# Kernel optimization log

Measured on AMD Instinct MI355X. Metric: run time of the kernel, lower is better.

## Reference

```python
import jax, jax.numpy as jnp
import numpy as np


def gcn_conv(x, W, b, src, dst):
    """PyG-style GCNConv: add self-loops, symmetric normalization, then scatter-add."""
    n = x.shape[0]
    loop = jnp.arange(n, dtype=src.dtype)
    s = jnp.concatenate([src, loop])  # [E+N]
    d = jnp.concatenate([dst, loop])
    deg = jax.ops.segment_sum(jnp.ones(s.shape[0], dtype=x.dtype), d, num_segments=n)
    dinv = jax.lax.rsqrt(jnp.maximum(deg, 1.0))  # deg >= 1 due to self-loops
    norm = dinv[s] * dinv[d]                     # [E+N]
    h = x @ W                                    # [N, out]
    msg = h[s] * norm[:, None]                   # gather + scale
    return jax.ops.segment_sum(msg, d, num_segments=n) + b


def setup_inputs() -> dict:
    key = jax.random.key(0)
    ks = jax.random.split(key, 8)
    N, E, IN, H, C = 50000, 800000, 128, 64, 16
    x = jax.random.normal(ks[0], (N, IN), dtype=jnp.float32)
    edge_index = jax.random.randint(ks[1], (2, E), 0, N, dtype=jnp.int32)
    def glorot(k, shp):
        fan_in, fan_out = shp
        lim = (6.0 / (fan_in + fan_out)) ** 0.5
        return jax.random.uniform(k, shp, jnp.float32, -lim, lim)
    return {
        "x": x,
        "edge_index": edge_index,
        "W1": glorot(ks[2], (IN, H)), "b1": jnp.zeros((H,), jnp.float32),
        "W2": glorot(ks[3], (H, H)),  "b2": jnp.zeros((H,), jnp.float32),
        "Wm1": glorot(ks[4], (2 * H, H)), "bm1": jnp.zeros((H,), jnp.float32),
        "Wm2": glorot(ks[5], (H, C)),     "bm2": jnp.zeros((C,), jnp.float32),
    }


def reference(x, edge_index, W1, b1, W2, b2, Wm1, bm1, Wm2, bm2):
    src, dst = edge_index[0], edge_index[1]
    h = jax.nn.relu(gcn_conv(x, W1, b1, src, dst))
    # dropout is identity in eval mode
    h = jax.nn.relu(gcn_conv(h, W2, b2, src, dst))
    ef = jnp.concatenate([h[src], h[dst]], axis=1)  # [E, 2H]
    z = jax.nn.relu(ef @ Wm1 + bm1)
    return z @ Wm2 + bm2  # [E, numClasses]
```

## Files before the change

### kernel.cpp

```cpp
#include <hip/hip_runtime.h>
#include <hip/hip_bf16.h>

__global__ __launch_bounds__(256) void k_deg(const int* __restrict__ dst, int* __restrict__ deg, int E) {
    int e = blockIdx.x * 256 + threadIdx.x;
    if (e < E) atomicAdd(&deg[dst[e]], 1);
}

__global__ __launch_bounds__(256) void k_dinv(const int* __restrict__ deg, float* __restrict__ dinv, int N) {
    int n = blockIdx.x * 256 + threadIdx.x;
    if (n < N) dinv[n] = rsqrtf((float)(deg[n] + 1));
}

__global__ __launch_bounds__(256) void k_scan_sum(const int* __restrict__ deg, int* __restrict__ bsum, int N) {
    int n = blockIdx.x * 256 + threadIdx.x;
    int v = (n < N) ? deg[n] : 0;
#pragma unroll
    for (int o = 32; o > 0; o >>= 1) v += __shfl_down(v, o, 64);
    __shared__ int sh[4];
    if ((threadIdx.x & 63) == 0) sh[threadIdx.x >> 6] = v;
    __syncthreads();
    if (threadIdx.x == 0) bsum[blockIdx.x] = sh[0] + sh[1] + sh[2] + sh[3];
}

__global__ __launch_bounds__(256) void k_scan_off(int* __restrict__ bsum, int nb) {
    __shared__ int sh[256];
    int t = threadIdx.x;
    sh[t] = (t < nb) ? bsum[t] : 0;
    __syncthreads();
    for (int o = 1; o < 256; o <<= 1) {
        int y = (t >= o) ? sh[t - o] : 0;
        __syncthreads();
        sh[t] += y;
        __syncthreads();
    }
    if (t < nb) bsum[t] = (t == 0) ? 0 : sh[t - 1];
}

__global__ __launch_bounds__(256) void k_scan_write(const int* __restrict__ deg, const int* __restrict__ boff,
                                                    int* __restrict__ row_start, int* __restrict__ cursor, int N) {
    int n = blockIdx.x * 256 + threadIdx.x;
    int t = threadIdx.x, lane = t & 63, w = t >> 6;
    int v = (n < N) ? deg[n] : 0;
    int x = v;
#pragma unroll
    for (int o = 1; o < 64; o <<= 1) {
        int y = __shfl_up(x, o, 64);
        if (lane >= o) x += y;
    }
    __shared__ int wsum[4];
    if (lane == 63) wsum[w] = x;
    __syncthreads();
    int wo = 0;
#pragma unroll
    for (int i = 0; i < 4; ++i) wo += (i < w) ? wsum[i] : 0;
    int excl = boff[blockIdx.x] + wo + x - v;
    if (n < N) { row_start[n] = excl; cursor[n] = excl; }
    if (n == N - 1) row_start[N] = excl + v;
}

template <bool PAIR>
__global__ __launch_bounds__(256) void k_fill(const int* __restrict__ src, const int* __restrict__ dst,
                                              int* __restrict__ cursor, void* __restrict__ item, int E) {
    int e = blockIdx.x * 256 + threadIdx.x;
    if (e < E) {
        int d = dst[e];
        int pos = atomicAdd(&cursor[d], 1);
        if (PAIR) ((int2*)item)[pos] = make_int2(src[e], e);
        else      ((int*)item)[pos] = e;
    }
}

__global__ __launch_bounds__(256) void k_tr(const float* __restrict__ in, float* __restrict__ outp, int R, int C) {
    int i = blockIdx.x * 256 + threadIdx.x;
    if (i < R * C) {
        int r = i / C, c = i % C;
        outp[(size_t)c * R + r] = in[(size_t)r * C + c];
    }
}

__global__ __launch_bounds__(256) void k_wpq(const float* __restrict__ Wm1, float* __restrict__ WPQ) {
    int i = blockIdx.x * 256 + threadIdx.x;
    if (i < 128 * 64) {
        int j = i >> 6, k = i & 63;
        WPQ[i] = (j < 64) ? Wm1[k * 64 + j] : Wm1[(64 + k) * 64 + (j - 64)];
    }
}

template <int K, bool RELU, bool BIAS>
__global__ __launch_bounds__(256) void k_mm_slice(const float* __restrict__ X,
                                                  const float* __restrict__ WT,
                                                  const float* __restrict__ bias,
                                                  float* __restrict__ Y, int N) {
    int n = blockIdx.x * 256 + threadIdx.x;
    int j0 = blockIdx.y * 16;
    int nc = n < N ? n : N - 1;
    const float* xr = X + (size_t)nc * K;
    const float* wr = WT + (size_t)j0 * K;
    float acc[16];
#pragma unroll
    for (int j = 0; j < 16; ++j) acc[j] = BIAS ? bias[j0 + j] : 0.f;
#pragma unroll 1
    for (int k0 = 0; k0 < K; k0 += 8) {
        float ef[8];
        *(float4*)(ef)     = *(const float4*)(xr + k0);
        *(float4*)(ef + 4) = *(const float4*)(xr + k0 + 4);
        if (RELU) {
#pragma unroll
            for (int kk = 0; kk < 8; ++kk) ef[kk] = fmaxf(ef[kk], 0.f);
        }
#pragma unroll
        for (int j = 0; j < 16; ++j) {
#pragma unroll
            for (int kk = 0; kk < 8; ++kk)
                acc[j] = fmaf(ef[kk], wr[j * K + k0 + kk], acc[j]);
        }
    }
    if (n < N) {
        float4* yp = (float4*)(Y + (size_t)n * 64 + j0);
#pragma unroll
        for (int q = 0; q < 4; ++q) yp[q] = *(float4*)(acc + q * 4);
    }
}

template <bool PAIR>
__global__ __launch_bounds__(256) void k_gather(const float* __restrict__ h, const float* __restrict__ dinv,
                                                const int* __restrict__ row_start, const void* __restrict__ item,
                                                const int* __restrict__ srcArr,
                                                const float* __restrict__ bias,
                                                float* __restrict__ a, int N) {
    int w = threadIdx.x >> 6, lane = threadIdx.x & 63;
    int d = blockIdx.x * 4 + w;
    if (d >= N) return;
    int beg = row_start[d], end = row_start[d + 1];
    float dd = dinv[d];
    float acc = fmaf(h[(size_t)d * 64 + lane], dd * dd, bias[lane]);
    int k = beg;
    for (; k + 4 <= end; k += 4) {
        int s0, s1, s2, s3;
        if (PAIR) {
            const int2* it = (const int2*)item;
            int2 p0 = it[k], p1 = it[k + 1], p2 = it[k + 2], p3 = it[k + 3];
            s0 = p0.x; s1 = p1.x; s2 = p2.x; s3 = p3.x;
        } else {
            const int* eid = (const int*)item;
            int e0 = eid[k], e1 = eid[k + 1], e2 = eid[k + 2], e3 = eid[k + 3];
            s0 = srcArr[e0]; s1 = srcArr[e1]; s2 = srcArr[e2]; s3 = srcArr[e3];
        }
        float n0 = dinv[s0] * dd, n1 = dinv[s1] * dd;
        float n2 = dinv[s2] * dd, n3 = dinv[s3] * dd;
        float v0 = h[(size_t)s0 * 64 + lane], v1 = h[(size_t)s1 * 64 + lane];
        float v2 = h[(size_t)s2 * 64 + lane], v3 = h[(size_t)s3 * 64 + lane];
        acc = fmaf(v0, n0, acc);
        acc = fmaf(v1, n1, acc);
        acc = fmaf(v2, n2, acc);
        acc = fmaf(v3, n3, acc);
    }
    for (; k < end; ++k) {
        int s;
        if (PAIR) s = ((const int2*)item)[k].x;
        else      s = srcArr[((const int*)item)[k]];
        acc = fmaf(h[(size_t)s * 64 + lane], dinv[s] * dd, acc);
    }
    a[(size_t)d * 64 + lane] = acc;
}

__global__ __launch_bounds__(256) void k_p_inplace(float* __restrict__ A2P,
                                                   const float* __restrict__ WPQ,
                                                   const float* __restrict__ bm1, int N) {
    int n = blockIdx.x * 256 + threadIdx.x;
    int nc = n < N ? n : N - 1;
    const float* xr = A2P + (size_t)nc * 64;
    float acc[64];
#pragma unroll
    for (int j = 0; j < 64; ++j) acc[j] = bm1[j];
#pragma unroll 1
    for (int k0 = 0; k0 < 64; k0 += 8) {
        float ef[8];
        *(float4*)(ef)     = *(const float4*)(xr + k0);
        *(float4*)(ef + 4) = *(const float4*)(xr + k0 + 4);
#pragma unroll
        for (int kk = 0; kk < 8; ++kk) ef[kk] = fmaxf(ef[kk], 0.f);
#pragma unroll
        for (int j = 0; j < 64; ++j)
#pragma unroll
            for (int kk = 0; kk < 8; ++kk)
                acc[j] = fmaf(ef[kk], WPQ[j * 64 + k0 + kk], acc[j]);
    }
    if (n < N) {
#pragma unroll
        for (int q = 0; q < 16; ++q)
            *(float4*)(A2P + (size_t)n * 64 + q * 4) = *(float4*)(acc + q * 4);
    }
}

__global__ __launch_bounds__(256) void k_edge_pq(const float* __restrict__ P,
                                                 const float* __restrict__ Q,
                                                 const int* __restrict__ src,
                                                 const int* __restrict__ dst,
                                                 const float* __restrict__ W2T,
                                                 const float* __restrict__ bm2,
                                                 float* __restrict__ out, int E) {
    int e = blockIdx.x * 256 + threadIdx.x;
    int ec = e < E ? e : E - 1;
    int s = src[ec], d = dst[ec];
    const float4* p4 = (const float4*)(P + (size_t)s * 64);
    const float4* q4 = (const float4*)(Q + (size_t)d * 64);
    float z[64];
#pragma unroll
    for (int c = 0; c < 16; ++c) {
        float4 a = p4[c], b = q4[c];
        z[c * 4 + 0] = fmaxf(a.x + b.x, 0.f);
        z[c * 4 + 1] = fmaxf(a.y + b.y, 0.f);
        z[c * 4 + 2] = fmaxf(a.z + b.z, 0.f);
        z[c * 4 + 3] = fmaxf(a.w + b.w, 0.f);
    }
    float o[16];
#pragma unroll
    for (int c = 0; c < 16; ++c) {
        float a = bm2[c];
#pragma unroll
        for (int j = 0; j < 64; ++j) a = fmaf(z[j], W2T[c * 64 + j], a);
        o[c] = a;
    }
    if (e < E) {
        float4* op = (float4*)(out + (size_t)e * 16);
#pragma unroll
        for (int q = 0; q < 4; ++q) op[q] = *(float4*)(o + q * 4);
    }
}

template <bool PAIR>
__global__ __launch_bounds__(256) void k_edge_csr(const float* __restrict__ P,
                                                  const float* __restrict__ Q,
                                                  const int* __restrict__ rowst,
                                                  const void* __restrict__ item,
                                                  const int* __restrict__ srcArr,
                                                  const float* __restrict__ W2T,
                                                  const float* __restrict__ bm2,
                                                  float* __restrict__ out, int E, int N) {
    int i = blockIdx.x * 256 + threadIdx.x;
    int ic = i < E ? i : E - 1;
    int s, e;
    if (PAIR) {
        int2 pe = ((const int2*)item)[ic];
        s = pe.x; e = pe.y;
    } else {
        e = ((const int*)item)[ic];
        s = srcArr[e];
    }
    int lo = 0, hi = N - 1;
    while (lo < hi) {
        int mid = (lo + hi + 1) >> 1;
        if (rowst[mid] <= ic) lo = mid; else hi = mid - 1;
    }
    const float4* p4 = (const float4*)(P + (size_t)s * 64);
    const float4* q4 = (const float4*)(Q + (size_t)lo * 64);
    float z[64];
#pragma unroll
    for (int c = 0; c < 16; ++c) {
        float4 a = p4[c], b = q4[c];
        z[c * 4 + 0] = fmaxf(a.x + b.x, 0.f);
        z[c * 4 + 1] = fmaxf(a.y + b.y, 0.f);
        z[c * 4 + 2] = fmaxf(a.z + b.z, 0.f);
        z[c * 4 + 3] = fmaxf(a.w + b.w, 0.f);
    }
    float o[16];
#pragma unroll
    for (int c = 0; c < 16; ++c) {
        float a = bm2[c];
#pragma unroll
        for (int j = 0; j < 64; ++j) a = fmaf(z[j], W2T[c * 64 + j], a);
        o[c] = a;
    }
    if (i < E) {
        float4* op = (float4*)(out + (size_t)e * 16);
#pragma unroll
        for (int q = 0; q < 4; ++q) op[q] = *(float4*)(o + q * 4);
    }
}

extern "C" void kernel_launch(void* const* d_in, const int* in_sizes, int n_in,
                              void* d_out, int out_size, void* d_ws, size_t ws_size,
                              hipStream_t stream) {
    const float* x   = (const float*)d_in[0];
    const int* ei    = (const int*)d_in[1];
    const float* W1  = (const float*)d_in[2];
    const float* b1  = (const float*)d_in[3];
    const float* W2  = (const float*)d_in[4];
    const float* b2  = (const float*)d_in[5];
    const float* Wm1 = (const float*)d_in[6];
    const float* bm1 = (const float*)d_in[7];
    const float* Wm2 = (const float*)d_in[8];
    const float* bm2 = (const float*)d_in[9];
    float* out = (float*)d_out;

    const int H  = in_sizes[3];
    const int IN = in_sizes[2] / H;
    const int N  = in_sizes[0] / IN;
    const int E  = in_sizes[1] / 2;
    const int* src = ei;
    const int* dst = ei + E;

    auto al = [](size_t b) { return (b + 255) & ~(size_t)255; };
    char* ws = (char*)d_ws;

    const size_t wb     = al((size_t)IN * H * 4) + al((size_t)H * H * 4) + al((size_t)2 * H * H * 4) + al((size_t)H * 16 * 4);
    const size_t rowstB = al(((size_t)N + 1) * 4);
    const size_t nodeB  = al((size_t)N * 64 * 4);
    const size_t pairB  = al((size_t)E * 8);
    const size_t eidB   = al((size_t)E * 4);
    const size_t needA  = wb + rowstB + pairB + 3 * nodeB;
    const size_t needB  = wb + rowstB + eidB  + 3 * nodeB;

    const int tier = (needA <= ws_size) ? 0 : (needB <= ws_size) ? 1 : 2;

    float *W1T, *W2T, *WPQ, *Wm2T, *bufB, *Qbuf, *Pbuf, *dinv;
    int *deg, *rowst, *cursor, *bsum;
    void* item;
    float* bufA = (float*)d_out;
    bool slicedP = true;

    size_t off = 0;
    auto alc = [&](size_t b) { void* p = ws + off; off += al(b); return p; };

    if (tier <= 1) {
        W1T  = (float*)alc((size_t)IN * H * 4);
        W2T  = (float*)alc((size_t)H * H * 4);
        WPQ  = (float*)alc((size_t)2 * H * H * 4);
        Wm2T = (float*)alc((size_t)H * 16 * 4);
        rowst = (int*)alc(((size_t)N + 1) * 4);
        item  = alc(tier == 0 ? (size_t)E * 8 : (size_t)E * 4);
        bufB = (float*)alc((size_t)N * 64 * 4);
        Qbuf = (float*)alc((size_t)N * 64 * 4);
        Pbuf = (float*)alc((size_t)N * 64 * 4);
        char* pz = (char*)Pbuf;
        dinv   = (float*)pz;
        deg    = (int*)(pz + al((size_t)N * 4));
        cursor = (int*)(pz + 2 * al((size_t)N * 4));
        bsum   = (int*)(pz + 3 * al((size_t)N * 4));
    } else {
        dinv = (float*)alc((size_t)N * 4);
        W1T  = (float*)alc((size_t)IN * H * 4);
        W2T  = (float*)alc((size_t)H * H * 4);
        WPQ  = (float*)alc((size_t)2 * H * H * 4);
        Wm2T = (float*)alc((size_t)H * 16 * 4);
        bufB = (float*)alc((size_t)N * 64 * 4);
        Qbuf = (float*)alc((size_t)N * 64 * 4);
        float* PbufSep = (float*)alc((size_t)N * 64 * 4);
        slicedP = (off <= ws_size);
        Pbuf = slicedP ? PbufSep : bufB;
        char* qz = (char*)Qbuf;
        size_t qo = 0;
        deg    = (int*)(qz + qo); qo += al((size_t)N * 4);
        rowst  = (int*)(qz + qo); qo += al(((size_t)N + 1) * 4);
        cursor = (int*)(qz + qo); qo += al((size_t)N * 4);
        bsum   = (int*)(qz + qo); qo += al(1024);
        item   = (void*)(qz + qo);
    }

    const int NBn = (N + 255) / 256;
    const int NBe = (E + 255) / 256;
    const int NG  = (N + 3) / 4;

    hipMemsetAsync(deg, 0, (size_t)N * sizeof(int), stream);
    k_deg<<<NBe, 256, 0, stream>>>(dst, deg, E);
    k_dinv<<<NBn, 256, 0, stream>>>(deg, dinv, N);
    k_scan_sum<<<NBn, 256, 0, stream>>>(deg, bsum, N);
    k_scan_off<<<1, 256, 0, stream>>>(bsum, NBn);
    k_scan_write<<<NBn, 256, 0, stream>>>(deg, bsum, rowst, cursor, N);
    if (tier == 1) k_fill<false><<<NBe, 256, 0, stream>>>(src, dst, cursor, item, E);
    else           k_fill<true ><<<NBe, 256, 0, stream>>>(src, dst, cursor, item, E);

    k_tr<<<(IN * H + 255) / 256, 256, 0, stream>>>(W1, W1T, IN, H);
    k_tr<<<(H * H + 255) / 256, 256, 0, stream>>>(W2, W2T, H, H);
    k_tr<<<(H * 16 + 255) / 256, 256, 0, stream>>>(Wm2, Wm2T, H, 16);
    k_wpq<<<(2 * H * H + 255) / 256, 256, 0, stream>>>(Wm1, WPQ);

    const dim3 G4(NBn, 4);

    k_mm_slice<128, false, false><<<G4, 256, 0, stream>>>(x, W1T, nullptr, bufA, N);
    if (tier == 1) k_gather<false><<<NG, 256, 0, stream>>>(bufA, dinv, rowst, item, src, b1, bufB, N);
    else           k_gather<true ><<<NG, 256, 0, stream>>>(bufA, dinv, rowst, item, src, b1, bufB, N);

    k_mm_slice<64, true, false><<<G4, 256, 0, stream>>>(bufB, W2T, nullptr, bufA, N);
    if (tier == 1) k_gather<false><<<NG, 256, 0, stream>>>(bufA, dinv, rowst, item, src, b2, bufB, N);
    else           k_gather<true ><<<NG, 256, 0, stream>>>(bufA, dinv, rowst, item, src, b2, bufB, N);

    k_mm_slice<64, true, false><<<G4, 256, 0, stream>>>(bufB, WPQ + 64 * 64, nullptr, Qbuf, N);
    if (slicedP) k_mm_slice<64, true, true><<<G4, 256, 0, stream>>>(bufB, WPQ, bm1, Pbuf, N);
    else         k_p_inplace<<<NBn, 256, 0, stream>>>(bufB, WPQ, bm1, N);

    if (tier == 0)      k_edge_csr<true ><<<NBe, 256, 0, stream>>>(Pbuf, Qbuf, rowst, item, src, Wm2T, bm2, out, E, N);
    else if (tier == 1) k_edge_csr<false><<<NBe, 256, 0, stream>>>(Pbuf, Qbuf, rowst, item, src, Wm2T, bm2, out, E, N);
    else                k_edge_pq<<<NBe, 256, 0, stream>>>(Pbuf, Qbuf, src, dst, Wm2T, bm2, out, E);
}
```

Baseline: 431.6 us.

## Prescale GCN features by dinv, replace binary search with dst vector, fuse P/Q matmuls

The GEMM epilogue now multiplies rows by dinv[n], so the gather loop only sums prescaled neighbour rows (unrolled by 8) and applies dd and the bias once at the end. This removes the per-edge dinv loads and multiplies. The edge kernel no longer binary-searches row_start for each edge. It reads a per-CSR-slot destination vector written by a new k_dvec kernel into bufB, and folds the ReLU'd z values straight into the 16 outputs without a 64-float array. The P and Q projections are merged into one launch over an 8-wide grid. In exchange it adds a kernel launch, writes E ints, and reuses bufB as scratch.

```diff
diff --git a/kernel.cpp b/kernel.cpp
--- a/kernel.cpp
+++ b/kernel.cpp
@@ -70,6 +70,14 @@
     }
 }
 
+__global__ __launch_bounds__(256) void k_dvec(const int* __restrict__ rowst, int* __restrict__ dvec, int N) {
+    int w = threadIdx.x >> 6, lane = threadIdx.x & 63;
+    int d = blockIdx.x * 4 + w;
+    if (d >= N) return;
+    int beg = rowst[d], end = rowst[d + 1];
+    for (int k = beg + lane; k < end; k += 64) dvec[k] = d;
+}
+
 __global__ __launch_bounds__(256) void k_tr(const float* __restrict__ in, float* __restrict__ outp, int R, int C) {
     int i = blockIdx.x * 256 + threadIdx.x;
     if (i < R * C) {
@@ -86,10 +94,11 @@
     }
 }
 
-template <int K, bool RELU, bool BIAS>
+template <int K, bool RELU, bool BIAS, bool SCALE>
 __global__ __launch_bounds__(256) void k_mm_slice(const float* __restrict__ X,
                                                   const float* __restrict__ WT,
                                                   const float* __restrict__ bias,
+                                                  const float* __restrict__ dinv,
                                                   float* __restrict__ Y, int N) {
     int n = blockIdx.x * 256 + threadIdx.x;
     int j0 = blockIdx.y * 16;
@@ -116,14 +125,54 @@
         }
     }
     if (n < N) {
+        if (SCALE) {
+            float dn = dinv[n];
+#pragma unroll
+            for (int j = 0; j < 16; ++j) acc[j] *= dn;
+        }
         float4* yp = (float4*)(Y + (size_t)n * 64 + j0);
 #pragma unroll
         for (int q = 0; q < 4; ++q) yp[q] = *(float4*)(acc + q * 4);
     }
 }
 
+__global__ __launch_bounds__(256) void k_pq_slice(const float* __restrict__ A2,
+                                                  const float* __restrict__ WPQ,
+                                                  const float* __restrict__ bm1,
+                                                  float* __restrict__ Pb, float* __restrict__ Qb, int N) {
+    int n = blockIdx.x * 256 + threadIdx.x;
+    int j0g = blockIdx.y * 16;
+    bool isP = j0g < 64;
+    int jo = isP ? j0g : j0g - 64;
+    float* Y = isP ? Pb : Qb;
+    int nc = n < N ? n : N - 1;
+    const float* xr = A2 + (size_t)nc * 64;
+    const float* wr = WPQ + (size_t)j0g * 64;
+    float acc[16];
+#pragma unroll
+    for (int j = 0; j < 16; ++j) acc[j] = isP ? bm1[jo + j] : 0.f;
+#pragma unroll 1
+    for (int k0 = 0; k0 < 64; k0 += 8) {
+        float ef[8];
+        *(float4*)(ef)     = *(const float4*)(xr + k0);
+        *(float4*)(ef + 4) = *(const float4*)(xr + k0 + 4);
+#pragma unroll
+        for (int kk = 0; kk < 8; ++kk) ef[kk] = fmaxf(ef[kk], 0.f);
+#pragma unroll
+        for (int j = 0; j < 16; ++j)
+#pragma unroll
+            for (int kk = 0; kk < 8; ++kk)
+                acc[j] = fmaf(ef[kk], wr[j * 64 + k0 + kk], acc[j]);
+    }
+    if (n < N) {
+        float4* yp = (float4*)(Y + (size_t)n * 64 + jo);
+#pragma unroll
+        for (int q = 0; q < 4; ++q) yp[q] = *(float4*)(acc + q * 4);
+    }
+}
+
 template <bool PAIR>
-__global__ __launch_bounds__(256) void k_gather(const float* __restrict__ h, const float* __restrict__ dinv,
+__global__ __launch_bounds__(256) void k_gather(const float* __restrict__ hs, const float* __restrict__ dinv,
                                                 const int* __restrict__ row_start, const void* __restrict__ item,
                                                 const int* __restrict__ srcArr,
                                                 const float* __restrict__ bias,
@@ -133,35 +182,33 @@
     if (d >= N) return;
     int beg = row_start[d], end = row_start[d + 1];
     float dd = dinv[d];
-    float acc = fmaf(h[(size_t)d * 64 + lane], dd * dd, bias[lane]);
+    float acc = hs[(size_t)d * 64 + lane];
     int k = beg;
-    for (; k + 4 <= end; k += 4) {
-        int s0, s1, s2, s3;
+    for (; k + 8 <= end; k += 8) {
+        int ss[8];
         if (PAIR) {
             const int2* it = (const int2*)item;
-            int2 p0 = it[k], p1 = it[k + 1], p2 = it[k + 2], p3 = it[k + 3];
-            s0 = p0.x; s1 = p1.x; s2 = p2.x; s3 = p3.x;
+#pragma unroll
+            for (int u = 0; u < 8; ++u) ss[u] = it[k + u].x;
         } else {
             const int* eid = (const int*)item;
-            int e0 = eid[k], e1 = eid[k + 1], e2 = eid[k + 2], e3 = eid[k + 3];
-            s0 = srcArr[e0]; s1 = srcArr[e1]; s2 = srcArr[e2]; s3 = srcArr[e3];
+            int ee[8];
+#pragma unroll
+            for (int u = 0; u < 8; ++u) ee[u] = eid[k + u];
+#pragma unroll
+            for (int u = 0; u < 8; ++u) ss[u] = srcArr[ee[u]];
         }
-        float n0 = dinv[s0] * dd, n1 = dinv[s1] * dd;
-        float n2 = dinv[s2] * dd, n3 = dinv[s3] * dd;
-        float v0 = h[(size_t)s0 * 64 + lane], v1 = h[(size_t)s1 * 64 + lane];
-        float v2 = h[(size_t)s2 * 64 + lane], v3 = h[(size_t)s3 * 64 + lane];
-        acc = fmaf(v0, n0, acc);
-        acc = fmaf(v1, n1, acc);
-        acc = fmaf(v2, n2, acc);
-        acc = fmaf(v3, n3, acc);
+        float v[8];
+#pragma unroll
+        for (int u = 0; u < 8; ++u) v[u] = hs[(size_t)ss[u] * 64 + lane];
+#pragma unroll
+        for (int u = 0; u < 8; ++u) acc += v[u];
     }
     for (; k < end; ++k) {
-        int s;
-        if (PAIR) s = ((const int2*)item)[k].x;
-        else      s = srcArr[((const int*)item)[k]];
-        acc = fmaf(h[(size_t)s * 64 + lane], dinv[s] * dd, acc);
-    }
-    a[(size_t)d * 64 + lane] = acc;
+        int s = PAIR ? ((const int2*)item)[k].x : srcArr[((const int*)item)[k]];
+        acc += hs[(size_t)s * 64 + lane];
+    }
+    a[(size_t)d * 64 + lane] = fmaf(acc, dd, bias[lane]);
 }
 
 __global__ __launch_bounds__(256) void k_p_inplace(float* __restrict__ A2P,
@@ -232,12 +279,12 @@
 template <bool PAIR>
 __global__ __launch_bounds__(256) void k_edge_csr(const float* __restrict__ P,
                                                   const float* __restrict__ Q,
-                                                  const int* __restrict__ rowst,
+                                                  const int* __restrict__ dvec,
                                                   const void* __restrict__ item,
                                                   const int* __restrict__ srcArr,
                                                   const float* __restrict__ W2T,
                                                   const float* __restrict__ bm2,
-                                                  float* __restrict__ out, int E, int N) {
+                                                  float* __restrict__ out, int E) {
     int i = blockIdx.x * 256 + threadIdx.x;
     int ic = i < E ? i : E - 1;
     int s, e;
@@ -248,29 +295,26 @@
         e = ((const int*)item)[ic];
         s = srcArr[e];
     }
-    int lo = 0, hi = N - 1;
-    while (lo < hi) {
-        int mid = (lo + hi + 1) >> 1;
-        if (rowst[mid] <= ic) lo = mid; else hi = mid - 1;
-    }
+    int d = dvec[ic];
     const float4* p4 = (const float4*)(P + (size_t)s * 64);
-    const float4* q4 = (const float4*)(Q + (size_t)lo * 64);
-    float z[64];
+    const float4* q4 = (const float4*)(Q + (size_t)d * 64);
+    float o[16];
+#pragma unroll
+    for (int t = 0; t < 16; ++t) o[t] = bm2[t];
 #pragma unroll
     for (int c = 0; c < 16; ++c) {
         float4 a = p4[c], b = q4[c];
-        z[c * 4 + 0] = fmaxf(a.x + b.x, 0.f);
-        z[c * 4 + 1] = fmaxf(a.y + b.y, 0.f);
-        z[c * 4 + 2] = fmaxf(a.z + b.z, 0.f);
-        z[c * 4 + 3] = fmaxf(a.w + b.w, 0.f);
-    }
-    float o[16];
-#pragma unroll
-    for (int c = 0; c < 16; ++c) {
-        float a = bm2[c];
-#pragma unroll
-        for (int j = 0; j < 64; ++j) a = fmaf(z[j], W2T[c * 64 + j], a);
-        o[c] = a;
+        float z0 = fmaxf(a.x + b.x, 0.f);
+        float z1 = fmaxf(a.y + b.y, 0.f);
+        float z2 = fmaxf(a.z + b.z, 0.f);
+        float z3 = fmaxf(a.w + b.w, 0.f);
+#pragma unroll
+        for (int t = 0; t < 16; ++t) {
+            o[t] = fmaf(z0, W2T[t * 64 + c * 4 + 0], o[t]);
+            o[t] = fmaf(z1, W2T[t * 64 + c * 4 + 1], o[t]);
+            o[t] = fmaf(z2, W2T[t * 64 + c * 4 + 2], o[t]);
+            o[t] = fmaf(z3, W2T[t * 64 + c * 4 + 3], o[t]);
+        }
     }
     if (i < E) {
         float4* op = (float4*)(out + (size_t)e * 16);
@@ -377,20 +421,26 @@
     k_wpq<<<(2 * H * H + 255) / 256, 256, 0, stream>>>(Wm1, WPQ);
 
     const dim3 G4(NBn, 4);
-
-    k_mm_slice<128, false, false><<<G4, 256, 0, stream>>>(x, W1T, nullptr, bufA, N);
+    const dim3 G8(NBn, 8);
+
+    k_mm_slice<128, false, false, true><<<G4, 256, 0, stream>>>(x, W1T, nullptr, dinv, bufA, N);
     if (tier == 1) k_gather<false><<<NG, 256, 0, stream>>>(bufA, dinv, rowst, item, src, b1, bufB, N);
     else           k_gather<true ><<<NG, 256, 0, stream>>>(bufA, dinv, rowst, item, src, b1, bufB, N);
 
-    k_mm_slice<64, true, false><<<G4, 256, 0, stream>>>(bufB, W2T, nullptr, bufA, N);
+    k_mm_slice<64, true, false, true><<<G4, 256, 0, stream>>>(bufB, W2T, nullptr, dinv, bufA, N);
     if (tier == 1) k_gather<false><<<NG, 256, 0, stream>>>(bufA, dinv, rowst, item, src, b2, bufB, N);
     else           k_gather<true ><<<NG, 256, 0, stream>>>(bufA, dinv, rowst, item, src, b2, bufB, N);
 
-    k_mm_slice<64, true, false><<<G4, 256, 0, stream>>>(bufB, WPQ + 64 * 64, nullptr, Qbuf, N);
-    if (slicedP) k_mm_slice<64, true, true><<<G4, 256, 0, stream>>>(bufB, WPQ, bm1, Pbuf, N);
-    else         k_p_inplace<<<NBn, 256, 0, stream>>>(bufB, WPQ, bm1, N);
-
-    if (tier == 0)      k_edge_csr<true ><<<NBe, 256, 0, stream>>>(Pbuf, Qbuf, rowst, item, src, Wm2T, bm2, out, E, N);
-    else if (tier == 1) k_edge_csr<false><<<NBe, 256, 0, stream>>>(Pbuf, Qbuf, rowst, item, src, Wm2T, bm2, out, E, N);
-    else                k_edge_pq<<<NBe, 256, 0, stream>>>(Pbuf, Qbuf, src, dst, Wm2T, bm2, out, E);
-}
+    if (tier <= 1) {
+        k_pq_slice<<<G8, 256, 0, stream>>>(bufB, WPQ, bm1, Pbuf, Qbuf, N);
+        int* dvec = (int*)bufB;
+        k_dvec<<<NG, 256, 0, stream>>>(rowst, dvec, N);
+        if (tier == 0) k_edge_csr<true ><<<NBe, 256, 0, stream>>>(Pbuf, Qbuf, dvec, item, src, Wm2T, bm2, out, E);
+        else           k_edge_csr<false><<<NBe, 256, 0, stream>>>(Pbuf, Qbuf, dvec, item, src, Wm2T, bm2, out, E);
+    } else {
+        k_mm_slice<64, true, false, false><<<G4, 256, 0, stream>>>(bufB, WPQ + 64 * 64, nullptr, nullptr, Qbuf, N);
+        if (slicedP) k_mm_slice<64, true, true, false><<<G4, 256, 0, stream>>>(bufB, WPQ, bm1, nullptr, Pbuf, N);
+        else         k_p_inplace<<<NBn, 256, 0, stream>>>(bufB, WPQ, bm1, N);
+        k_edge_pq<<<NBe, 256, 0, stream>>>(Pbuf, Qbuf, src, dst, Wm2T, bm2, out, E);
+    }
+}
```

Result: no change. 424.6 us (-1.6%).
